# Performance work log

Hardware: AMD Instinct MI355X
Metric: run time of the kernel (lower is better)

The kernel has to match this reference:

```python
import jax, jax.numpy as jnp
import numpy as np

N_EMB = 1024
N_HEAD = 16
HEAD_DIM = N_EMB // N_HEAD


def setup_inputs() -> dict:
    key = jax.random.key(0)
    k_x, k_wa, k_ba, k_wp, k_bp = jax.random.split(key, 5)
    B, S = 4, 2048
    scale = 1.0 / np.sqrt(N_EMB)
    return {
        "x": jax.random.normal(k_x, (B, S, N_EMB), dtype=jnp.float32),
        "W_attn": jax.random.normal(k_wa, (N_EMB, 3 * N_EMB), dtype=jnp.float32) * scale,
        "b_attn": jax.random.normal(k_ba, (3 * N_EMB,), dtype=jnp.float32) * 0.01,
        "W_proj": jax.random.normal(k_wp, (N_EMB, N_EMB), dtype=jnp.float32) * scale,
        "b_proj": jax.random.normal(k_bp, (N_EMB,), dtype=jnp.float32) * 0.01,
    }


def _attention(x, W_attn, b_attn, W_proj, b_proj):
    B, S, E = x.shape
    qkv = x @ W_attn + b_attn  # [B, S, 3E]
    q, k, v = jnp.split(qkv, 3, axis=-1)
    # [B, H, S, D]
    q = q.reshape(B, S, N_HEAD, HEAD_DIM).transpose(0, 2, 1, 3)
    k = k.reshape(B, S, N_HEAD, HEAD_DIM).transpose(0, 2, 1, 3)
    v = v.reshape(B, S, N_HEAD, HEAD_DIM).transpose(0, 2, 1, 3)
    scores = jnp.einsum("bhqd,bhkd->bhqk", q, k) / jnp.sqrt(jnp.asarray(HEAD_DIM, x.dtype))
    causal = jnp.tril(jnp.ones((S, S), dtype=bool))
    scores = jnp.where(causal, scores, jnp.asarray(-jnp.inf, x.dtype))
    probs = jax.nn.softmax(scores, axis=-1)
    y = jnp.einsum("bhqk,bhkd->bhqd", probs, v)  # [B, H, S, D]
    y = y.transpose(0, 2, 1, 3).reshape(B, S, E)
    return y @ W_proj + b_proj


def reference(x, W_attn, b_attn, W_proj, b_proj):
    return _attention(x, W_attn, b_attn, W_proj, b_proj)
```

## Files before the change

### kernel.cpp

```cpp
#include <hip/hip_runtime.h>
#include <hip/hip_bf16.h>

typedef __bf16 bf16x8 __attribute__((ext_vector_type(8)));
typedef __bf16 bf16x4 __attribute__((ext_vector_type(4)));
typedef float f32x4 __attribute__((ext_vector_type(4)));

#define MFMA16(a, b, c) __builtin_amdgcn_mfma_f32_16x16x32_bf16(a, b, c, 0, 0, 0)

#define BATCH 4
#define SEQ   2048
#define EMB   1024
#define NHEAD 16
#define HDIM  64
#define ROWS  (BATCH * SEQ)
#define N_QKV (3 * EMB)
#define BH_STRIDE (SEQ * HDIM)

__device__ __forceinline__ void gload_lds16(const __bf16* gp, __bf16* lp) {
  __builtin_amdgcn_global_load_lds(
      (const __attribute__((address_space(1))) void*)gp,
      (__attribute__((address_space(3))) void*)lp, 16, 0, 0);
}

__global__ void cast_f32_to_bf16_x4(const float* __restrict__ src,
                                    __bf16* __restrict__ dst, int n4) {
  int i = blockIdx.x * blockDim.x + threadIdx.x;
  if (i >= n4) return;
  float4 f = ((const float4*)src)[i];
  bf16x4 o;
  o.x = (__bf16)f.x; o.y = (__bf16)f.y; o.z = (__bf16)f.z; o.w = (__bf16)f.w;
  ((bf16x4*)dst)[i] = o;
}

__global__ void transpose_to_bf16(const float* __restrict__ src,
                                  __bf16* __restrict__ dst, int R, int C) {
  __shared__ float t[32][33];
  int c0 = blockIdx.x * 32, r0 = blockIdx.y * 32;
  int tx = threadIdx.x, ty = threadIdx.y;
#pragma unroll
  for (int i = 0; i < 32; i += 8)
    t[ty + i][tx] = src[(size_t)(r0 + ty + i) * C + c0 + tx];
  __syncthreads();
#pragma unroll
  for (int i = 0; i < 32; i += 8)
    dst[(size_t)(c0 + ty + i) * R + r0 + tx] = (__bf16)t[tx][ty + i];
}

__global__ __launch_bounds__(256) void gemm_qkv(
    const __bf16* __restrict__ A, const __bf16* __restrict__ Bt,
    const float* __restrict__ bias,
    __bf16* __restrict__ Qt, __bf16* __restrict__ Kt, __bf16* __restrict__ Vt) {
  const int K = EMB;
  __shared__ __align__(16) __bf16 sA[128 * 32];
  __shared__ __align__(16) __bf16 sB[128 * 32];
  int m0 = blockIdx.y * 128, n0 = blockIdx.x * 128;
  int tid = threadIdx.x;
  int wave = tid >> 6, lane = tid & 63;
  int wr = wave >> 1, wc = wave & 1;
  int l16 = lane & 15, quad = lane >> 4;
  int f1 = tid * 8;
  int r1 = f1 >> 5, c1 = f1 & 31;
  int f2 = f1 + 2048;
  int r2 = f2 >> 5, c2 = f2 & 31;
  f32x4 acc[4][4] = {};
  for (int k0 = 0; k0 < K; k0 += 32) {
    gload_lds16(A + (size_t)(m0 + r1) * K + k0 + c1, &sA[wave * 512]);
    gload_lds16(A + (size_t)(m0 + r2) * K + k0 + c2, &sA[2048 + wave * 512]);
    gload_lds16(Bt + (size_t)(n0 + r1) * K + k0 + c1, &sB[wave * 512]);
    gload_lds16(Bt + (size_t)(n0 + r2) * K + k0 + c2, &sB[2048 + wave * 512]);
    __syncthreads();
    bf16x8 a[4], b[4];
#pragma unroll
    for (int i = 0; i < 4; i++)
      a[i] = *(const bf16x8*)(sA + (wr * 64 + i * 16 + l16) * 32 + quad * 8);
#pragma unroll
    for (int j = 0; j < 4; j++)
      b[j] = *(const bf16x8*)(sB + (wc * 64 + j * 16 + l16) * 32 + quad * 8);
#pragma unroll
    for (int i = 0; i < 4; i++)
#pragma unroll
      for (int j = 0; j < 4; j++) acc[i][j] = MFMA16(a[i], b[j], acc[i][j]);
    __syncthreads();
  }
  const float KSC = 0.18033688011112043f;
  int sec = n0 >> 10;
#pragma unroll
  for (int i = 0; i < 4; i++) {
    int row = m0 + wr * 64 + i * 16 + quad * 4;
    int bidx = row >> 11;
    int srow = row & 2047;
#pragma unroll
    for (int j = 0; j < 4; j++) {
      int col = n0 + wc * 64 + j * 16 + l16;
      float bv = bias[col];
      int e = col & 1023;
      int h = e >> 6, d = e & 63;
      size_t base = (size_t)(bidx * NHEAD + h) * BH_STRIDE;
      if (sec == 0) {
        int idx = (srow >> 4) * 1024 + (d >> 5) * 512 + quad * 32 +
                  ((d >> 3) & 3) * 128 + (d & 7);
#pragma unroll
        for (int r = 0; r < 4; r++)
          Qt[base + idx + r * 8] = (__bf16)((acc[i][j][r] + bv) * KSC);
      } else if (sec == 1) {
        int idx = (srow >> 6) * 4096 + ((srow >> 4) & 3) * 1024 + (d >> 5) * 512 +
                  quad * 32 + ((d >> 3) & 3) * 128 + (d & 7);
#pragma unroll
        for (int r = 0; r < 4; r++)
          Kt[base + idx + r * 8] = (__bf16)(acc[i][j][r] + bv);
      } else {
        int idx = (srow >> 6) * 4096 + (d >> 4) * 1024 + ((srow >> 5) & 1) * 512 +
                  (d & 15) * 8 + (((i & 1) * 2 + (quad >> 1))) * 128 + (quad & 1) * 4;
        bf16x4 o4;
        o4.x = (__bf16)(acc[i][j][0] + bv);
        o4.y = (__bf16)(acc[i][j][1] + bv);
        o4.z = (__bf16)(acc[i][j][2] + bv);
        o4.w = (__bf16)(acc[i][j][3] + bv);
        *(bf16x4*)(Vt + base + idx) = o4;
      }
    }
  }
}

#define PS2 68
__global__ __launch_bounds__(256) void attn_fwd(
    const __bf16* __restrict__ Qt, const __bf16* __restrict__ Kt,
    const __bf16* __restrict__ Vt, __bf16* __restrict__ Y) {
  __shared__ __align__(16) __bf16 pbuf[4][16 * PS2];
  int id = blockIdx.x;
  int qb = id >> 6;
  int hb = id & 63;
  int h = hb >> 2, b = hb & 3;
  int wave = threadIdx.x >> 6, lane = threadIdx.x & 63;
  int l16 = lane & 15, quad = lane >> 4;
  int quad4 = quad * 4;
  int q0 = qb * 64;
  size_t bh = (size_t)b * NHEAD + h;
  const __bf16* Qh = Qt + bh * BH_STRIDE;
  const __bf16* Kh = Kt + bh * BH_STRIDE;
  const __bf16* Vh = Vt + bh * BH_STRIDE;
  int mq = q0 + wave * 16;
  const __bf16* qbase = Qh + (size_t)(mq >> 4) * 1024 + lane * 8;
  bf16x8 qf0 = *(const bf16x8*)(qbase);
  bf16x8 qf1 = *(const bf16x8*)(qbase + 512);
  f32x4 acc[4] = {};
  float l_part = 0.f;
  const float NEG_INF = -__builtin_inff();
  __bf16* pw = pbuf[wave];
  int kt_end = q0 + 64;
  bf16x8 ka[4], kb[4];
  {
    const __bf16* kp = Kh + lane * 8;
#pragma unroll
    for (int t = 0; t < 4; t++) {
      ka[t] = *(const bf16x8*)(kp + t * 1024);
      kb[t] = *(const bf16x8*)(kp + t * 1024 + 512);
    }
  }
  for (int kt = 0; kt < kt_end; kt += 64) {
    f32x4 st[4];
#pragma unroll
    for (int t = 0; t < 4; t++) {
      f32x4 z = {};
      z = MFMA16(ka[t], qf0, z);
      st[t] = MFMA16(kb[t], qf1, z);
    }
    {
      int ktn = kt + 64 < kt_end ? kt + 64 : kt;
      const __bf16* kp = Kh + (size_t)(ktn >> 6) * 4096 + lane * 8;
#pragma unroll
      for (int t = 0; t < 4; t++) {
        ka[t] = *(const bf16x8*)(kp + t * 1024);
        kb[t] = *(const bf16x8*)(kp + t * 1024 + 512);
      }
    }
    bf16x8 va[4], vb[4];
    {
      const __bf16* vp = Vh + (size_t)(kt >> 6) * 4096 + lane * 8;
#pragma unroll
      for (int jj = 0; jj < 4; jj++) {
        va[jj] = *(const bf16x8*)(vp + jj * 1024);
        vb[jj] = *(const bf16x8*)(vp + jj * 1024 + 512);
      }
    }
    float p[4][4];
    if (kt + 64 > mq) {
      int rel = mq + l16 - kt;
#pragma unroll
      for (int t = 0; t < 4; t++)
#pragma unroll
        for (int r = 0; r < 4; r++) {
          float x = st[t][r];
          if (t * 16 + quad4 + r > rel) x = NEG_INF;
          p[t][r] = exp2f(x);
        }
    } else {
#pragma unroll
      for (int t = 0; t < 4; t++)
#pragma unroll
        for (int r = 0; r < 4; r++) p[t][r] = exp2f(st[t][r]);
    }
    float ts[4];
#pragma unroll
    for (int t = 0; t < 4; t++)
      ts[t] = (p[t][0] + p[t][1]) + (p[t][2] + p[t][3]);
    l_part += (ts[0] + ts[1]) + (ts[2] + ts[3]);
#pragma unroll
    for (int t = 0; t < 4; t++) {
      bf16x4 o4;
      o4.x = (__bf16)p[t][0]; o4.y = (__bf16)p[t][1];
      o4.z = (__bf16)p[t][2]; o4.w = (__bf16)p[t][3];
      *(bf16x4*)(pw + l16 * PS2 + t * 16 + quad4) = o4;
    }
    bf16x8 pf0 = *(const bf16x8*)(pw + l16 * PS2 + quad * 8);
    bf16x8 pf1 = *(const bf16x8*)(pw + l16 * PS2 + 32 + quad * 8);
#pragma unroll
    for (int jj = 0; jj < 4; jj++) {
      acc[jj] = MFMA16(va[jj], pf0, acc[jj]);
      acc[jj] = MFMA16(vb[jj], pf1, acc[jj]);
    }
  }
  float lt = l_part;
  lt += __shfl_xor(lt, 16);
  lt += __shfl_xor(lt, 32);
  float inv = 1.f / lt;
  int gq = mq + l16;
#pragma unroll
  for (int jj = 0; jj < 4; jj++) {
    bf16x4 o4;
    o4.x = (__bf16)(acc[jj][0] * inv);
    o4.y = (__bf16)(acc[jj][1] * inv);
    o4.z = (__bf16)(acc[jj][2] * inv);
    o4.w = (__bf16)(acc[jj][3] * inv);
    *(bf16x4*)(Y + ((size_t)b * SEQ + gq) * EMB + h * HDIM + jj * 16 + quad4) = o4;
  }
}

__global__ __launch_bounds__(256) void gemm_proj(
    const __bf16* __restrict__ A, const __bf16* __restrict__ Bt,
    const float* __restrict__ bias, float* __restrict__ out) {
  const int K = EMB;
  __shared__ __align__(16) __bf16 sA[128 * 32];
  __shared__ __align__(16) __bf16 sB[128 * 32];
  int m0 = blockIdx.y * 128, n0 = blockIdx.x * 128;
  int tid = threadIdx.x;
  int wave = tid >> 6, lane = tid & 63;
  int wr = wave >> 1, wc = wave & 1;
  int l16 = lane & 15, quad = lane >> 4;
  int f1 = tid * 8;
  int r1 = f1 >> 5, c1 = f1 & 31;
  int f2 = f1 + 2048;
  int r2 = f2 >> 5, c2 = f2 & 31;
  f32x4 acc[4][4] = {};
  for (int k0 = 0; k0 < K; k0 += 32) {
    gload_lds16(A + (size_t)(m0 + r1) * K + k0 + c1, &sA[wave * 512]);
    gload_lds16(A + (size_t)(m0 + r2) * K + k0 + c2, &sA[2048 + wave * 512]);
    gload_lds16(Bt + (size_t)(n0 + r1) * K + k0 + c1, &sB[wave * 512]);
    gload_lds16(Bt + (size_t)(n0 + r2) * K + k0 + c2, &sB[2048 + wave * 512]);
    __syncthreads();
    bf16x8 a[4], b[4];
#pragma unroll
    for (int i = 0; i < 4; i++)
      a[i] = *(const bf16x8*)(sA + (wr * 64 + i * 16 + l16) * 32 + quad * 8);
#pragma unroll
    for (int j = 0; j < 4; j++)
      b[j] = *(const bf16x8*)(sB + (wc * 64 + j * 16 + l16) * 32 + quad * 8);
#pragma unroll
    for (int i = 0; i < 4; i++)
#pragma unroll
      for (int j = 0; j < 4; j++) acc[i][j] = MFMA16(a[i], b[j], acc[i][j]);
    __syncthreads();
  }
#pragma unroll
  for (int i = 0; i < 4; i++) {
    int row = m0 + wr * 64 + i * 16 + quad * 4;
#pragma unroll
    for (int j = 0; j < 4; j++) {
      int col = n0 + wc * 64 + j * 16 + l16;
      float bv = bias[col];
#pragma unroll
      for (int r = 0; r < 4; r++)
        out[(size_t)(row + r) * EMB + col] = acc[i][j][r] + bv;
    }
  }
}

extern "C" void kernel_launch(void* const* d_in, const int* in_sizes, int n_in,
                              void* d_out, int out_size, void* d_ws, size_t ws_size,
                              hipStream_t stream) {
  const float* x      = (const float*)d_in[0];
  const float* W_attn = (const float*)d_in[1];
  const float* b_attn = (const float*)d_in[2];
  const float* W_proj = (const float*)d_in[3];
  const float* b_proj = (const float*)d_in[4];
  float* out = (float*)d_out;

  char* ws = (char*)d_ws;
  size_t off = 0;
  __bf16* xb   = (__bf16*)(ws + off); off += (size_t)ROWS * EMB * 2;
  __bf16* Wa_t = (__bf16*)(ws + off); off += (size_t)N_QKV * EMB * 2;
  __bf16* Wp_t = (__bf16*)(ws + off); off += (size_t)EMB * EMB * 2;
  __bf16* Qt   = (__bf16*)(ws + off); off += (size_t)ROWS * EMB * 2;
  __bf16* Kt   = (__bf16*)(ws + off); off += (size_t)ROWS * EMB * 2;
  __bf16* Vt   = (__bf16*)(ws + off); off += (size_t)ROWS * EMB * 2;
  __bf16* Yb   = (__bf16*)(ws + off); off += (size_t)ROWS * EMB * 2;

  {
    int n4 = ROWS * EMB / 4;
    cast_f32_to_bf16_x4<<<(n4 + 255) / 256, 256, 0, stream>>>(x, xb, n4);
    dim3 blk(32, 8);
    transpose_to_bf16<<<dim3(N_QKV / 32, EMB / 32), blk, 0, stream>>>(W_attn, Wa_t, EMB, N_QKV);
    transpose_to_bf16<<<dim3(EMB / 32, EMB / 32), blk, 0, stream>>>(W_proj, Wp_t, EMB, EMB);
  }
  gemm_qkv<<<dim3(N_QKV / 128, ROWS / 128), 256, 0, stream>>>(xb, Wa_t, b_attn, Qt, Kt, Vt);
  attn_fwd<<<dim3(SEQ / 64 * NHEAD * BATCH), 256, 0, stream>>>(Qt, Kt, Vt, Yb);
  gemm_proj<<<dim3(EMB / 128, ROWS / 128), 256, 0, stream>>>(Yb, Wp_t, b_proj, out);
}
```

Measured before the change: 280.0 us.

## Remap GEMM blocks per XCD, trim attention registers, raise occupancy

Both GEMMs switch to a 1D grid whose block IDs are remapped so that consecutive blocks on each of the 8 XCDs cover neighbouring tiles, aiming for better L2 reuse. The attention kernel drops the K prefetch and the whole-tile V register buffers. It now loads K and V fragments just before each MFMA, uses the raw hardware exp2 builtin, and requests 8 blocks per CU through launch bounds. The goal is lower register pressure and higher occupancy, traded against losing software prefetch, so load latency must be hidden by other waves.

```diff
diff --git a/kernel.cpp b/kernel.cpp
--- a/kernel.cpp
+++ b/kernel.cpp
@@ -53,7 +53,10 @@
   const int K = EMB;
   __shared__ __align__(16) __bf16 sA[128 * 32];
   __shared__ __align__(16) __bf16 sB[128 * 32];
-  int m0 = blockIdx.y * 128, n0 = blockIdx.x * 128;
+  int id = blockIdx.x;
+  int lid = (id & 7) * (1536 >> 3) + (id >> 3);
+  int bx = lid % 24, by = lid / 24;
+  int m0 = by * 128, n0 = bx * 128;
   int tid = threadIdx.x;
   int wave = tid >> 6, lane = tid & 63;
   int wr = wave >> 1, wc = wave & 1;
@@ -123,7 +126,7 @@
 }
 
 #define PS2 68
-__global__ __launch_bounds__(256) void attn_fwd(
+__global__ __launch_bounds__(256, 8) void attn_fwd(
     const __bf16* __restrict__ Qt, const __bf16* __restrict__ Kt,
     const __bf16* __restrict__ Vt, __bf16* __restrict__ Y) {
   __shared__ __align__(16) __bf16 pbuf[4][16 * PS2];
@@ -148,76 +151,45 @@
   const float NEG_INF = -__builtin_inff();
   __bf16* pw = pbuf[wave];
   int kt_end = q0 + 64;
-  bf16x8 ka[4], kb[4];
-  {
-    const __bf16* kp = Kh + lane * 8;
+  for (int kt = 0; kt < kt_end; kt += 64) {
+    const __bf16* kp = Kh + (size_t)(kt >> 6) * 4096 + lane * 8;
+    bool diag = (kt + 64 > mq);
+    int rel = mq + l16 - kt;
 #pragma unroll
     for (int t = 0; t < 4; t++) {
-      ka[t] = *(const bf16x8*)(kp + t * 1024);
-      kb[t] = *(const bf16x8*)(kp + t * 1024 + 512);
-    }
-  }
-  for (int kt = 0; kt < kt_end; kt += 64) {
-    f32x4 st[4];
-#pragma unroll
-    for (int t = 0; t < 4; t++) {
+      bf16x8 ka = *(const bf16x8*)(kp + t * 1024);
+      bf16x8 kb = *(const bf16x8*)(kp + t * 1024 + 512);
       f32x4 z = {};
-      z = MFMA16(ka[t], qf0, z);
-      st[t] = MFMA16(kb[t], qf1, z);
-    }
-    {
-      int ktn = kt + 64 < kt_end ? kt + 64 : kt;
-      const __bf16* kp = Kh + (size_t)(ktn >> 6) * 4096 + lane * 8;
-#pragma unroll
-      for (int t = 0; t < 4; t++) {
-        ka[t] = *(const bf16x8*)(kp + t * 1024);
-        kb[t] = *(const bf16x8*)(kp + t * 1024 + 512);
+      z = MFMA16(ka, qf0, z);
+      z = MFMA16(kb, qf1, z);
+      float p0, p1, p2, p3;
+      if (diag) {
+        int kl = t * 16 + quad4;
+        p0 = __builtin_amdgcn_exp2f(kl + 0 > rel ? NEG_INF : z[0]);
+        p1 = __builtin_amdgcn_exp2f(kl + 1 > rel ? NEG_INF : z[1]);
+        p2 = __builtin_amdgcn_exp2f(kl + 2 > rel ? NEG_INF : z[2]);
+        p3 = __builtin_amdgcn_exp2f(kl + 3 > rel ? NEG_INF : z[3]);
+      } else {
+        p0 = __builtin_amdgcn_exp2f(z[0]);
+        p1 = __builtin_amdgcn_exp2f(z[1]);
+        p2 = __builtin_amdgcn_exp2f(z[2]);
+        p3 = __builtin_amdgcn_exp2f(z[3]);
       }
-    }
-    bf16x8 va[4], vb[4];
-    {
-      const __bf16* vp = Vh + (size_t)(kt >> 6) * 4096 + lane * 8;
-#pragma unroll
-      for (int jj = 0; jj < 4; jj++) {
-        va[jj] = *(const bf16x8*)(vp + jj * 1024);
-        vb[jj] = *(const bf16x8*)(vp + jj * 1024 + 512);
-      }
-    }
-    float p[4][4];
-    if (kt + 64 > mq) {
-      int rel = mq + l16 - kt;
-#pragma unroll
-      for (int t = 0; t < 4; t++)
-#pragma unroll
-        for (int r = 0; r < 4; r++) {
-          float x = st[t][r];
-          if (t * 16 + quad4 + r > rel) x = NEG_INF;
-          p[t][r] = exp2f(x);
-        }
-    } else {
-#pragma unroll
-      for (int t = 0; t < 4; t++)
-#pragma unroll
-        for (int r = 0; r < 4; r++) p[t][r] = exp2f(st[t][r]);
-    }
-    float ts[4];
-#pragma unroll
-    for (int t = 0; t < 4; t++)
-      ts[t] = (p[t][0] + p[t][1]) + (p[t][2] + p[t][3]);
-    l_part += (ts[0] + ts[1]) + (ts[2] + ts[3]);
-#pragma unroll
-    for (int t = 0; t < 4; t++) {
+      l_part += (p0 + p1) + (p2 + p3);
       bf16x4 o4;
-      o4.x = (__bf16)p[t][0]; o4.y = (__bf16)p[t][1];
-      o4.z = (__bf16)p[t][2]; o4.w = (__bf16)p[t][3];
+      o4.x = (__bf16)p0; o4.y = (__bf16)p1;
+      o4.z = (__bf16)p2; o4.w = (__bf16)p3;
       *(bf16x4*)(pw + l16 * PS2 + t * 16 + quad4) = o4;
     }
     bf16x8 pf0 = *(const bf16x8*)(pw + l16 * PS2 + quad * 8);
     bf16x8 pf1 = *(const bf16x8*)(pw + l16 * PS2 + 32 + quad * 8);
+    const __bf16* vp = Vh + (size_t)(kt >> 6) * 4096 + lane * 8;
 #pragma unroll
     for (int jj = 0; jj < 4; jj++) {
-      acc[jj] = MFMA16(va[jj], pf0, acc[jj]);
-      acc[jj] = MFMA16(vb[jj], pf1, acc[jj]);
+      bf16x8 va = *(const bf16x8*)(vp + jj * 1024);
+      bf16x8 vb = *(const bf16x8*)(vp + jj * 1024 + 512);
+      acc[jj] = MFMA16(va, pf0, acc[jj]);
+      acc[jj] = MFMA16(vb, pf1, acc[jj]);
     }
   }
   float lt = l_part;
@@ -242,7 +214,10 @@
   const int K = EMB;
   __shared__ __align__(16) __bf16 sA[128 * 32];
   __shared__ __align__(16) __bf16 sB[128 * 32];
-  int m0 = blockIdx.y * 128, n0 = blockIdx.x * 128;
+  int id = blockIdx.x;
+  int lid = (id & 7) * (512 >> 3) + (id >> 3);
+  int bx = lid & 7, by = lid >> 3;
+  int m0 = by * 128, n0 = bx * 128;
   int tid = threadIdx.x;
   int wave = tid >> 6, lane = tid & 63;
   int wr = wave >> 1, wc = wave & 1;
@@ -312,7 +287,7 @@
     transpose_to_bf16<<<dim3(N_QKV / 32, EMB / 32), blk, 0, stream>>>(W_attn, Wa_t, EMB, N_QKV);
     transpose_to_bf16<<<dim3(EMB / 32, EMB / 32), blk, 0, stream>>>(W_proj, Wp_t, EMB, EMB);
   }
-  gemm_qkv<<<dim3(N_QKV / 128, ROWS / 128), 256, 0, stream>>>(xb, Wa_t, b_attn, Qt, Kt, Vt);
+  gemm_qkv<<<dim3(1536), 256, 0, stream>>>(xb, Wa_t, b_attn, Qt, Kt, Vt);
   attn_fwd<<<dim3(SEQ / 64 * NHEAD * BATCH), 256, 0, stream>>>(Qt, Kt, Vt, Yb);
-  gemm_proj<<<dim3(EMB / 128, ROWS / 128), 256, 0, stream>>>(Yb, Wp_t, b_proj, out);
-}
+  gemm_proj<<<dim3(512), 256, 0, stream>>>(Yb, Wp_t, b_proj, out);
+}
```

After: 283.0 us. Within noise of the previous version (+1.1%).
